# Kernel optimization log

Measured on AMD Instinct MI355X. Metric: run time of the kernel, lower is better.

The kernel has to match this reference:

```python
import jax, jax.numpy as jnp
import numpy as np

D_MODEL = 128
NUM_LAYERS = 2
D_FF = 512
VOCAB = 128
OUT_DIM = 10
B, S = 512, 256
EPS_FEAT = 1e-6
LN_EPS = 1e-5


def _pos_encoding(seq_len, d):
    pos = jnp.arange(seq_len, dtype=jnp.float32)[:, None]            # [S,1]
    div = jnp.exp(jnp.arange(0, d, 2, dtype=jnp.float32) * (-np.log(10000.0) / d))
    ang = pos * div                                                   # [S,D/2]
    pe = jnp.stack([jnp.sin(ang), jnp.cos(ang)], axis=-1).reshape(seq_len, d)
    return pe[:, None, :]                                             # [S,1,D]


def _layer_norm(x, g, b):
    mu = jnp.mean(x, axis=-1, keepdims=True)
    var = jnp.mean(jnp.square(x - mu), axis=-1, keepdims=True)
    return (x - mu) * jax.lax.rsqrt(var + LN_EPS) * g + b


def setup_inputs() -> dict:
    key = jax.random.key(0)
    ks = jax.random.split(key, 20)
    sc = 0.02
    inp = {
        'src': jax.random.randint(ks[0], (B, S), 0, VOCAB),
        'emb': jax.random.normal(ks[1], (VOCAB, D_MODEL), jnp.float32) * sc,
        'wq': jax.random.normal(ks[2], (NUM_LAYERS, D_MODEL, D_MODEL), jnp.float32) * sc,
        'bq': jnp.zeros((NUM_LAYERS, D_MODEL), jnp.float32),
        'wk': jax.random.normal(ks[3], (NUM_LAYERS, D_MODEL, D_MODEL), jnp.float32) * sc,
        'bk': jnp.zeros((NUM_LAYERS, D_MODEL), jnp.float32),
        'wv': jax.random.normal(ks[4], (NUM_LAYERS, D_MODEL, D_MODEL), jnp.float32) * sc,
        'bv': jnp.zeros((NUM_LAYERS, D_MODEL), jnp.float32),
        'w1': jax.random.normal(ks[5], (NUM_LAYERS, D_FF, D_MODEL), jnp.float32) * sc,
        'b1': jnp.zeros((NUM_LAYERS, D_FF), jnp.float32),
        'w2': jax.random.normal(ks[6], (NUM_LAYERS, D_MODEL, D_FF), jnp.float32) * sc,
        'b2': jnp.zeros((NUM_LAYERS, D_MODEL), jnp.float32),
        'g1': jnp.ones((NUM_LAYERS, D_MODEL), jnp.float32),
        'beta1': jnp.zeros((NUM_LAYERS, D_MODEL), jnp.float32),
        'g2': jnp.ones((NUM_LAYERS, D_MODEL), jnp.float32),
        'beta2': jnp.zeros((NUM_LAYERS, D_MODEL), jnp.float32),
        'fc_w': jax.random.normal(ks[7], (OUT_DIM, D_MODEL), jnp.float32) * sc,
        'fc_b': jnp.zeros((OUT_DIM,), jnp.float32),
    }
    return inp


def reference(src, emb, wq, bq, wk, bk, wv, bv, w1, b1, w2, b2,
              g1, beta1, g2, beta2, fc_w, fc_b):
    # src: [B,S] int -> permute -> [S,B]
    x = emb[src.T] * np.sqrt(float(D_MODEL))          # [S,B,D]
    x = x + _pos_encoding(x.shape[0], D_MODEL)
    for l in range(NUM_LAYERS):
        # Linear attention (faithful to original: einsum 'b' axis = seq here)
        Q = jax.nn.relu(jnp.einsum('sbd,ed->sbe', x, wq[l]) + bq[l]) + EPS_FEAT
        K = jax.nn.relu(jnp.einsum('sbd,ed->sbe', x, wk[l]) + bk[l]) + EPS_FEAT
        V = jnp.einsum('sbd,ed->sbe', x, wv[l]) + bv[l]
        KV = jnp.einsum('snd,sne->sde', K, V)         # [S,D,D] (n = batch axis)
        Z = 1.0 / (jnp.einsum('snd,sd->sn', Q, K.sum(axis=1)) + EPS_FEAT)  # [S,B]
        attn = jnp.einsum('snd,sde,sn->sne', Q, KV, Z)  # [S,B,D]
        x = _layer_norm(x + attn, g1[l], beta1[l])
        ff = jnp.einsum('sbf,df->sbd',
                        jax.nn.relu(jnp.einsum('sbd,fd->sbf', x, w1[l]) + b1[l]),
                        w2[l]) + b2[l]
        x = _layer_norm(x + ff, g2[l], beta2[l])
    x = jnp.transpose(x, (1, 0, 2))                   # [B,S,D]
    pooled = jnp.mean(x, axis=1)                      # [B,D]
    return pooled @ fc_w.T + fc_b                     # [B,OUT]
```

## Files before the change

### kernel.cpp

```cpp
#include <hip/hip_runtime.h>

typedef unsigned short u16;
typedef unsigned int u32;
typedef short bf16x8 __attribute__((ext_vector_type(8)));
typedef float f32x4 __attribute__((ext_vector_type(4)));

__device__ __forceinline__ float b2f(u16 v) { return __uint_as_float(((u32)v) << 16); }
__device__ __forceinline__ u16 f2b(float f) {
    u32 x = __float_as_uint(f);
    return (u16)((x + 0x7fffu + ((x >> 16) & 1u)) >> 16);
}

#define S_LEN 256
#define B_SZ  512
#define DM    128
#define DFF   512
#define MROWS (S_LEN * B_SZ)

__device__ __forceinline__ int sw16(int r, int d) {
    return r * 128 + ((((d >> 3) ^ (r & 15)) & 15) << 3) + (d & 7);
}

__global__ __launch_bounds__(256) void detect_kernel(const u32* __restrict__ embw,
                                                     int* __restrict__ flag) {
    int z = 0, big = 0;
    for (int i = threadIdx.x; i < 8192; i += 256) {
        u32 w = embw[i];
        u32 lo = w & 0xffffu;
        if (lo == 0u) z++;
        else if (((lo >> 7) & 0xffu) >= 0xC0u) big++;
    }
#pragma unroll
    for (int off = 32; off > 0; off >>= 1) {
        z   += __shfl_xor(z, off, 64);
        big += __shfl_xor(big, off, 64);
    }
    __shared__ int zz[4], bb[4];
    if ((threadIdx.x & 63) == 0) { zz[threadIdx.x >> 6] = z; bb[threadIdx.x >> 6] = big; }
    __syncthreads();
    if (threadIdx.x == 0) {
        int Z = zz[0] + zz[1] + zz[2] + zz[3];
        int Bc = bb[0] + bb[1] + bb[2] + bb[3];
        flag[0] = (Z > 4096 || Bc > 16) ? 1 : 0;
    }
}

struct Ptrs { const void* p[17]; };

__global__ __launch_bounds__(256) void convert_kernel(Ptrs ps, u16* __restrict__ canon,
                                                      const int* __restrict__ flag) {
    const int cnt[17] = {16384,32768,256,32768,256,32768,256,131072,1024,131072,
                         256,256,256,256,256,1280,10};
    const int off[17] = {0,16384,49152,49408,82176,82432,115200,115456,246528,
                         247552,378624,378880,379136,379392,379648,379904,381184};
    const int bst[18] = {0,8,24,25,41,42,58,59,123,124,188,189,190,191,192,193,194,195};
    const int isf = *flag;
    const int blk = blockIdx.x;
    int idx = 0;
#pragma unroll
    for (int i = 0; i < 17; ++i) if (blk >= bst[i + 1]) idx = i + 1;
    const int local = blk - bst[idx];
    const int n = cnt[idx];
    const void* sp = ps.p[idx];
    u16* dp = canon + off[idx];
#pragma unroll
    for (int j = 0; j < 8; ++j) {
        int e = local * 2048 + j * 256 + threadIdx.x;
        if (e < n) {
            u16 v = isf ? f2b(((const float*)sp)[e]) : ((const u16*)sp)[e];
            dp[e] = v;
        }
    }
}

__global__ __launch_bounds__(256) void embed_kernel(const int* __restrict__ src,
                                                    const u16* __restrict__ emb,
                                                    u16* __restrict__ X) {
    int idx = blockIdx.x * 256 + threadIdx.x;
    int d2 = idx & 63;
    int m = idx >> 6;
    int s = m >> 9;
    int b = m & 511;
    int tok = src[b * S_LEN + s];
    int d = d2 * 2;
    float e0 = b2f(emb[tok * DM + d])     * 11.3137084989847604f;
    float e1 = b2f(emb[tok * DM + d + 1]) * 11.3137084989847604f;
    float ang = (float)s * expf((float)d * -0.0719557841560639f);
    float v0 = e0 + sinf(ang);
    float v1 = e1 + cosf(ang);
    u32 w = (u32)f2b(v0) | ((u32)f2b(v1) << 16);
    *(u32*)(X + (size_t)m * DM + d) = w;
}

__global__ __launch_bounds__(256) void kvproj_kernel(
    const u16* __restrict__ X, const u16* __restrict__ Wk, const u16* __restrict__ bk,
    const u16* __restrict__ Wv, const u16* __restrict__ bv,
    u16* __restrict__ KVt, float* __restrict__ Ksum)
{
    __shared__ __align__(16) char sm_[49152];
    u16* Xs = (u16*)sm_;
    u16* Kt = (u16*)(sm_ + 16384);
    u16* Vt = (u16*)(sm_ + 32768);
    const int s = blockIdx.x, t = threadIdx.x;
    const int w = t >> 6, quad = (t >> 4) & 3, lr = t & 15;
    const u16* Xg = X + (size_t)s * B_SZ * DM;

    bf16x8 wkf[2][4], wvf[2][4];
    float kb[2], vb[2];
#pragma unroll
    for (int ct = 0; ct < 2; ++ct) {
        int e = w * 32 + ct * 16 + lr;
#pragma unroll
        for (int kc = 0; kc < 4; ++kc) {
            wkf[ct][kc] = *(const bf16x8*)(Wk + e * 128 + kc * 32 + quad * 8);
            wvf[ct][kc] = *(const bf16x8*)(Wv + e * 128 + kc * 32 + quad * 8);
        }
        kb[ct] = b2f(bk[e]);
        vb[ct] = b2f(bv[e]);
    }

    const f32x4 z4 = {0.f, 0.f, 0.f, 0.f};
    f32x4 kvacc[2][8];
#pragma unroll
    for (int dt = 0; dt < 2; ++dt)
#pragma unroll
        for (int ct = 0; ct < 8; ++ct) kvacc[dt][ct] = z4;
    float ks[2] = {0.f, 0.f};

    for (int b0 = 0; b0 < B_SZ; b0 += 64) {
        __syncthreads();
#pragma unroll
        for (int i = 0; i < 4; ++i) {
            int e8 = (i * 256 + t) * 8; int r = e8 >> 7, k0 = e8 & 127;
            *(uint4*)(Xs + sw16(r, k0)) = *(const uint4*)(Xg + (size_t)(b0 + r) * DM + k0);
        }
        __syncthreads();
        f32x4 pa[4][2];
#pragma unroll
        for (int mt = 0; mt < 4; ++mt) { pa[mt][0] = z4; pa[mt][1] = z4; }
#pragma unroll
        for (int kc = 0; kc < 4; ++kc) {
            bf16x8 a[4];
#pragma unroll
            for (int mt = 0; mt < 4; ++mt)
                a[mt] = *(const bf16x8*)(Xs + sw16(mt * 16 + lr, kc * 32 + quad * 8));
#pragma unroll
            for (int ct = 0; ct < 2; ++ct)
#pragma unroll
                for (int mt = 0; mt < 4; ++mt)
                    pa[mt][ct] = __builtin_amdgcn_mfma_f32_16x16x32_bf16(a[mt], wkf[ct][kc], pa[mt][ct], 0, 0, 0);
        }
#pragma unroll
        for (int ct = 0; ct < 2; ++ct) {
            int e = w * 32 + ct * 16 + lr, e7 = e & 7;
#pragma unroll
            for (int mt = 0; mt < 4; ++mt) {
                u16 h[4]; float ssum = 0.f;
#pragma unroll
                for (int j = 0; j < 4; ++j) {
                    float v = fmaxf(pa[mt][ct][j] + kb[ct], 0.f) + 1e-6f;
                    h[j] = f2b(v); ssum += b2f(h[j]);
                }
                ks[ct] += ssum;
                uint2 pk; pk.x = (u32)h[0] | ((u32)h[1] << 16); pk.y = (u32)h[2] | ((u32)h[3] << 16);
                int bs = mt * 2 + (quad >> 1);
                *(uint2*)(Kt + e * 64 + (((bs ^ e7) & 7) << 3) + (quad & 1) * 4) = pk;
            }
        }
#pragma unroll
        for (int mt = 0; mt < 4; ++mt) { pa[mt][0] = z4; pa[mt][1] = z4; }
#pragma unroll
        for (int kc = 0; kc < 4; ++kc) {
            bf16x8 a[4];
#pragma unroll
            for (int mt = 0; mt < 4; ++mt)
                a[mt] = *(const bf16x8*)(Xs + sw16(mt * 16 + lr, kc * 32 + quad * 8));
#pragma unroll
            for (int ct = 0; ct < 2; ++ct)
#pragma unroll
                for (int mt = 0; mt < 4; ++mt)
                    pa[mt][ct] = __builtin_amdgcn_mfma_f32_16x16x32_bf16(a[mt], wvf[ct][kc], pa[mt][ct], 0, 0, 0);
        }
#pragma unroll
        for (int ct = 0; ct < 2; ++ct) {
            int e = w * 32 + ct * 16 + lr, e7 = e & 7;
#pragma unroll
            for (int mt = 0; mt < 4; ++mt) {
                u16 h[4];
#pragma unroll
                for (int j = 0; j < 4; ++j) h[j] = f2b(pa[mt][ct][j] + vb[ct]);
                uint2 pk; pk.x = (u32)h[0] | ((u32)h[1] << 16); pk.y = (u32)h[2] | ((u32)h[3] << 16);
                int bs = mt * 2 + (quad >> 1);
                *(uint2*)(Vt + e * 64 + (((bs ^ e7) & 7) << 3) + (quad & 1) * 4) = pk;
            }
        }
        __syncthreads();
#pragma unroll
        for (int kc = 0; kc < 2; ++kc) {
            bf16x8 ka[2];
#pragma unroll
            for (int dt = 0; dt < 2; ++dt) {
                int d = (2 * w + dt) * 16 + lr;
                ka[dt] = *(const bf16x8*)(Kt + d * 64 + ((((kc * 4 + quad) ^ (d & 7)) & 7) << 3));
            }
#pragma unroll
            for (int ct = 0; ct < 8; ++ct) {
                int e = ct * 16 + lr;
                bf16x8 vf = *(const bf16x8*)(Vt + e * 64 + ((((kc * 4 + quad) ^ (e & 7)) & 7) << 3));
                kvacc[0][ct] = __builtin_amdgcn_mfma_f32_16x16x32_bf16(ka[0], vf, kvacc[0][ct], 0, 0, 0);
                kvacc[1][ct] = __builtin_amdgcn_mfma_f32_16x16x32_bf16(ka[1], vf, kvacc[1][ct], 0, 0, 0);
            }
        }
    }
#pragma unroll
    for (int ct = 0; ct < 2; ++ct) {
        float v = ks[ct];
        v += __shfl_xor(v, 16, 64);
        v += __shfl_xor(v, 32, 64);
        if (quad == 0) Ksum[s * 128 + w * 32 + ct * 16 + lr] = v;
    }
    u16* KVg = KVt + (size_t)s * (DM * DM);
#pragma unroll
    for (int dt = 0; dt < 2; ++dt) {
        int d0 = (2 * w + dt) * 16 + quad * 4;
#pragma unroll
        for (int ct = 0; ct < 8; ++ct) {
            int e = ct * 16 + lr;
            u16 h[4];
#pragma unroll
            for (int j = 0; j < 4; ++j) h[j] = f2b(kvacc[dt][ct][j]);
            uint2 pk; pk.x = (u32)h[0] | ((u32)h[1] << 16); pk.y = (u32)h[2] | ((u32)h[3] << 16);
            *(uint2*)(KVg + e * 128 + d0) = pk;
        }
    }
}

__global__ __launch_bounds__(256, 2) void attn_mlp_kernel(
    const u16* X, const u16* __restrict__ Wq, const u16* __restrict__ bq,
    const u16* __restrict__ KVt, const float* __restrict__ Ksum,
    const u16* __restrict__ W1, const u16* __restrict__ b1,
    const u16* __restrict__ W2, const u16* __restrict__ b2,
    u16* Xout,
    const u16* __restrict__ g1v_, const u16* __restrict__ be1_,
    const u16* __restrict__ g2v_, const u16* __restrict__ be2_)
{
    __shared__ __align__(16) char sm_[81920];
    u16* R1  = (u16*)sm_;
    u16* R2  = (u16*)(sm_ + 32768);
    u16* Hc  = (u16*)(sm_ + 65536);
    u16* W1c = R1;
    u16* W2c = R1 + 8192;
    u16* Out = R1;
    const int blk = blockIdx.x, s = blk >> 2, rc = blk & 3, t = threadIdx.x;
    const int w = t >> 6, quad = (t >> 4) & 3, lr = t & 15;
    const size_t m0 = (size_t)s * B_SZ + rc * 128;

#pragma unroll
    for (int i = 0; i < 8; ++i) {
        int e8 = (i * 256 + t) * 8; int r = e8 >> 7, k0 = e8 & 127;
        *(uint4*)(R1 + sw16(r, k0)) = *(const uint4*)(Wq + e8);
        *(uint4*)(R2 + sw16(r, k0)) = *(const uint4*)(X + (m0 + r) * DM + k0);
    }
    __syncthreads();
    const f32x4 z4 = {0.f, 0.f, 0.f, 0.f};
    f32x4 qacc[2][8];
#pragma unroll
    for (int mt = 0; mt < 2; ++mt)
#pragma unroll
        for (int ct = 0; ct < 8; ++ct) qacc[mt][ct] = z4;
#pragma unroll
    for (int kc = 0; kc < 4; ++kc) {
        bf16x8 a[2];
#pragma unroll
        for (int mt = 0; mt < 2; ++mt)
            a[mt] = *(const bf16x8*)(R2 + sw16(w * 32 + mt * 16 + lr, kc * 32 + quad * 8));
#pragma unroll
        for (int ct = 0; ct < 8; ++ct) {
            bf16x8 wf = *(const bf16x8*)(R1 + sw16(ct * 16 + lr, kc * 32 + quad * 8));
            qacc[0][ct] = __builtin_amdgcn_mfma_f32_16x16x32_bf16(a[0], wf, qacc[0][ct], 0, 0, 0);
            qacc[1][ct] = __builtin_amdgcn_mfma_f32_16x16x32_bf16(a[1], wf, qacc[1][ct], 0, 0, 0);
        }
    }
    __syncthreads();
    float ksm[8], bqv[8];
#pragma unroll
    for (int ct = 0; ct < 8; ++ct) {
        ksm[ct] = Ksum[s * 128 + ct * 16 + lr];
        bqv[ct] = b2f(bq[ct * 16 + lr]);
    }
    float zden[2][4];
#pragma unroll
    for (int mt = 0; mt < 2; ++mt)
#pragma unroll
        for (int j = 0; j < 4; ++j) zden[mt][j] = 0.f;
#pragma unroll
    for (int mt = 0; mt < 2; ++mt)
#pragma unroll
        for (int ct = 0; ct < 8; ++ct) {
            int d = ct * 16 + lr;
#pragma unroll
            for (int j = 0; j < 4; ++j) {
                float qv = fmaxf(qacc[mt][ct][j] + bqv[ct], 0.f) + 1e-6f;
                u16 qb16 = f2b(qv);
                zden[mt][j] += b2f(qb16) * ksm[ct];
                int b = w * 32 + mt * 16 + quad * 4 + j;
                R1[sw16(b, d)] = qb16;
            }
        }
#pragma unroll
    for (int mt = 0; mt < 2; ++mt)
#pragma unroll
        for (int j = 0; j < 4; ++j) {
            float v = zden[mt][j];
            v += __shfl_xor(v, 1, 64); v += __shfl_xor(v, 2, 64);
            v += __shfl_xor(v, 4, 64); v += __shfl_xor(v, 8, 64);
            zden[mt][j] = 1.f / (v + 1e-6f);
        }
    const u16* KVg = KVt + (size_t)s * (DM * DM);
#pragma unroll
    for (int i = 0; i < 8; ++i) {
        int e8 = (i * 256 + t) * 8; int r = e8 >> 7, k0 = e8 & 127;
        *(uint4*)(R2 + sw16(r, k0)) = *(const uint4*)(KVg + e8);
    }
    __syncthreads();
    f32x4 oacc[2][8];
#pragma unroll
    for (int mt = 0; mt < 2; ++mt)
#pragma unroll
        for (int ct = 0; ct < 8; ++ct) oacc[mt][ct] = z4;
#pragma unroll
    for (int kc = 0; kc < 4; ++kc) {
        bf16x8 qa[2];
#pragma unroll
        for (int mt = 0; mt < 2; ++mt)
            qa[mt] = *(const bf16x8*)(R1 + sw16(w * 32 + mt * 16 + lr, kc * 32 + quad * 8));
#pragma unroll
        for (int ct = 0; ct < 8; ++ct) {
            bf16x8 kf = *(const bf16x8*)(R2 + sw16(ct * 16 + lr, kc * 32 + quad * 8));
            oacc[0][ct] = __builtin_amdgcn_mfma_f32_16x16x32_bf16(qa[0], kf, oacc[0][ct], 0, 0, 0);
            oacc[1][ct] = __builtin_amdgcn_mfma_f32_16x16x32_bf16(qa[1], kf, oacc[1][ct], 0, 0, 0);
        }
    }
    __syncthreads();
    {
        float gv[8], bev[8];
#pragma unroll
        for (int ct = 0; ct < 8; ++ct) {
            gv[ct]  = b2f(g1v_[ct * 16 + lr]);
            bev[ct] = b2f(be1_[ct * 16 + lr]);
        }
#pragma unroll
        for (int mt = 0; mt < 2; ++mt)
#pragma unroll
            for (int j = 0; j < 4; ++j) {
                int b = w * 32 + mt * 16 + quad * 4 + j;
                const u16* xr = X + (m0 + b) * DM;
                float vals[8], sum = 0.f, sq = 0.f;
#pragma unroll
                for (int ct = 0; ct < 8; ++ct) {
                    float v = fmaf(oacc[mt][ct][j], zden[mt][j], b2f(xr[ct * 16 + lr]));
                    vals[ct] = v; sum += v; sq += v * v;
                }
                sum += __shfl_xor(sum, 1, 64); sq += __shfl_xor(sq, 1, 64);
                sum += __shfl_xor(sum, 2, 64); sq += __shfl_xor(sq, 2, 64);
                sum += __shfl_xor(sum, 4, 64); sq += __shfl_xor(sq, 4, 64);
                sum += __shfl_xor(sum, 8, 64); sq += __shfl_xor(sq, 8, 64);
                float mean = sum * 0.0078125f;
                float var  = sq * 0.0078125f - mean * mean;
                float rstd = rsqrtf(fmaxf(var, 0.f) + 1e-5f);
#pragma unroll
                for (int ct = 0; ct < 8; ++ct)
                    R2[sw16(b, ct * 16 + lr)] =
                        f2b((vals[ct] - mean) * rstd * gv[ct] + bev[ct]);
            }
    }
    bf16x8 xf[2][4];
#pragma unroll
    for (int mt = 0; mt < 2; ++mt)
#pragma unroll
        for (int kc = 0; kc < 4; ++kc)
            xf[mt][kc] = *(const bf16x8*)(R2 + sw16(w * 32 + mt * 16 + lr, kc * 32 + quad * 8));

    f32x4 zacc[2][8];
#pragma unroll
    for (int mt = 0; mt < 2; ++mt)
#pragma unroll
        for (int ct = 0; ct < 8; ++ct) zacc[mt][ct] = z4;

    for (int fc = 0; fc < DFF; fc += 64) {
        __syncthreads();
#pragma unroll
        for (int i = 0; i < 4; ++i) {
            int e8 = (i * 256 + t) * 8; int r = e8 >> 7, k0 = e8 & 127;
            *(uint4*)(W1c + sw16(r, k0)) = *(const uint4*)(W1 + (size_t)(fc + r) * DM + k0);
        }
#pragma unroll
        for (int i = 0; i < 4; ++i) {
            int e8 = (i * 256 + t) * 8; int d = e8 >> 6, f0 = e8 & 63;
            *(uint4*)(W2c + d * 64 + ((((f0 >> 3) ^ (d & 7)) & 7) << 3)) =
                *(const uint4*)(W2 + (size_t)d * DFF + fc + f0);
        }
        __syncthreads();
        f32x4 hacc[2][4];
#pragma unroll
        for (int mt = 0; mt < 2; ++mt)
#pragma unroll
            for (int ct = 0; ct < 4; ++ct) hacc[mt][ct] = z4;
#pragma unroll
        for (int kc = 0; kc < 4; ++kc) {
#pragma unroll
            for (int ct = 0; ct < 4; ++ct) {
                bf16x8 wa = *(const bf16x8*)(W1c + sw16(ct * 16 + lr, kc * 32 + quad * 8));
                hacc[0][ct] = __builtin_amdgcn_mfma_f32_16x16x32_bf16(wa, xf[0][kc], hacc[0][ct], 0, 0, 0);
                hacc[1][ct] = __builtin_amdgcn_mfma_f32_16x16x32_bf16(wa, xf[1][kc], hacc[1][ct], 0, 0, 0);
            }
        }
#pragma unroll
        for (int ct = 0; ct < 4; ++ct) {
            float hb[4];
#pragma unroll
            for (int j = 0; j < 4; ++j) hb[j] = b2f(b1[fc + ct * 16 + quad * 4 + j]);
#pragma unroll
            for (int mt = 0; mt < 2; ++mt) {
                int m = w * 32 + mt * 16 + lr;
                u16 h[4];
#pragma unroll
                for (int j = 0; j < 4; ++j)
                    h[j] = f2b(fmaxf(hacc[mt][ct][j] + hb[j], 0.f));
                uint2 pk; pk.x = (u32)h[0] | ((u32)h[1] << 16);
                pk.y = (u32)h[2] | ((u32)h[3] << 16);
                int slot = (ct * 2 + (quad >> 1)) ^ (m & 7);
                *(uint2*)(Hc + m * 64 + (slot << 3) + (quad & 1) * 4) = pk;
            }
        }
#pragma unroll
        for (int kc = 0; kc < 2; ++kc) {
            bf16x8 ha[2];
#pragma unroll
            for (int mt = 0; mt < 2; ++mt) {
                int m = w * 32 + mt * 16 + lr;
                ha[mt] = *(const bf16x8*)(Hc + m * 64 + ((((kc * 4 + quad) ^ (m & 7)) & 7) << 3));
            }
#pragma unroll
            for (int ct = 0; ct < 8; ++ct) {
                int d = ct * 16 + lr;
                bf16x8 wb = *(const bf16x8*)(W2c + d * 64 + ((((kc * 4 + quad) ^ (d & 7)) & 7) << 3));
                zacc[0][ct] = __builtin_amdgcn_mfma_f32_16x16x32_bf16(ha[0], wb, zacc[0][ct], 0, 0, 0);
                zacc[1][ct] = __builtin_amdgcn_mfma_f32_16x16x32_bf16(ha[1], wb, zacc[1][ct], 0, 0, 0);
            }
        }
    }
    __syncthreads();
    {
        float gv[8], bev[8], b2v[8];
#pragma unroll
        for (int ct = 0; ct < 8; ++ct) {
            gv[ct]  = b2f(g2v_[ct * 16 + lr]);
            bev[ct] = b2f(be2_[ct * 16 + lr]);
            b2v[ct] = b2f(b2[ct * 16 + lr]);
        }
#pragma unroll
        for (int mt = 0; mt < 2; ++mt)
#pragma unroll
            for (int j = 0; j < 4; ++j) {
                int r = w * 32 + mt * 16 + quad * 4 + j;
                float vals[8], sum = 0.f, sq = 0.f;
#pragma unroll
                for (int ct = 0; ct < 8; ++ct) {
                    float v = zacc[mt][ct][j] + b2v[ct] + b2f(R2[sw16(r, ct * 16 + lr)]);
                    vals[ct] = v; sum += v; sq += v * v;
                }
                sum += __shfl_xor(sum, 1, 64); sq += __shfl_xor(sq, 1, 64);
                sum += __shfl_xor(sum, 2, 64); sq += __shfl_xor(sq, 2, 64);
                sum += __shfl_xor(sum, 4, 64); sq += __shfl_xor(sq, 4, 64);
                sum += __shfl_xor(sum, 8, 64); sq += __shfl_xor(sq, 8, 64);
                float mean = sum * 0.0078125f;
                float var  = sq * 0.0078125f - mean * mean;
                float rstd = rsqrtf(fmaxf(var, 0.f) + 1e-5f);
#pragma unroll
                for (int ct = 0; ct < 8; ++ct)
                    Out[r * 128 + ct * 16 + lr] =
                        f2b((vals[ct] - mean) * rstd * gv[ct] + bev[ct]);
            }
    }
    __syncthreads();
#pragma unroll
    for (int i = 0; i < 8; ++i) {
        int e8 = (i * 256 + t) * 8; int r = e8 >> 7, k0 = e8 & 127;
        uint4 v = *(const uint4*)(Out + r * 128 + k0);
        *(uint4*)(Xout + (m0 + r) * DM + k0) = v;
    }
}

__global__ __launch_bounds__(128) void pool_fc_kernel(
    const u16* __restrict__ X, const u16* __restrict__ fcw,
    const u16* __restrict__ fcb, void* __restrict__ Out,
    const int* __restrict__ flag)
{
    __shared__ float pool[128];
    const int b = blockIdx.x, t = threadIdx.x;
    float acc = 0.f;
    for (int s = 0; s < S_LEN; ++s)
        acc += b2f(X[((size_t)s * B_SZ + b) * DM + t]);
    pool[t] = acc * (1.0f / 256.0f);
    __syncthreads();
    if (t < 10) {
        float o = b2f(fcb[t]);
        for (int d = 0; d < 128; ++d) o += pool[d] * b2f(fcw[t * 128 + d]);
        if (*flag) ((float*)Out)[b * 10 + t] = o;
        else       ((u16*)Out)[b * 10 + t] = f2b(o);
    }
}

extern "C" void kernel_launch(void* const* d_in, const int* in_sizes, int n_in,
                              void* d_out, int out_size, void* d_ws, size_t ws_size,
                              hipStream_t stream)
{
    const int* src = (const int*)d_in[0];

    char* ws = (char*)d_ws;
    u16*   X    = (u16*)ws;
    u16*   KVt  = (u16*)(ws + 33554432);
    float* Ksum = (float*)(ws + 41943040);
    int*   flag = (int*)(ws + 42074112);
    u16*   cn   = (u16*)(ws + 42074368);

    u16* emb = cn + 0;
    u16* wq  = cn + 16384;
    u16* bq  = cn + 49152;
    u16* wk  = cn + 49408;
    u16* bk  = cn + 82176;
    u16* wv  = cn + 82432;
    u16* bvp = cn + 115200;
    u16* w1  = cn + 115456;
    u16* b1  = cn + 246528;
    u16* w2  = cn + 247552;
    u16* b2  = cn + 378624;
    u16* g1  = cn + 378880;
    u16* be1 = cn + 379136;
    u16* g2  = cn + 379392;
    u16* be2 = cn + 379648;
    u16* fcw = cn + 379904;
    u16* fcb = cn + 381184;

    detect_kernel<<<1, 256, 0, stream>>>((const u32*)d_in[1], flag);

    Ptrs ps;
    for (int i = 0; i < 17; ++i) ps.p[i] = d_in[i + 1];
    convert_kernel<<<195, 256, 0, stream>>>(ps, cn, flag);

    embed_kernel<<<MROWS * 64 / 256, 256, 0, stream>>>(src, emb, X);

    for (int l = 0; l < 2; ++l) {
        kvproj_kernel<<<S_LEN, 256, 0, stream>>>(
            X, wk + l * DM * DM, bk + l * DM, wv + l * DM * DM, bvp + l * DM, KVt, Ksum);
        attn_mlp_kernel<<<S_LEN * 4, 256, 0, stream>>>(
            X, wq + l * DM * DM, bq + l * DM, KVt, Ksum,
            w1 + l * DFF * DM, b1 + l * DFF, w2 + l * DM * DFF, b2 + l * DM,
            X, g1 + l * DM, be1 + l * DM, g2 + l * DM, be2 + l * DM);
    }

    pool_fc_kernel<<<B_SZ, 128, 0, stream>>>(X, fcw, fcb, d_out, flag);
}
```

Before: 450.4 us.

## Register-prefetch X, KV, and FFN weight tiles to overlap global loads with MFMA

Adds register double-buffering. The next X tile in the KV kernel, the KV matrix in the attention/FFN kernel, and the next W1/W2 chunk in the FFN loop are now loaded from global memory into registers while MFMA work on the current tile runs, then stored into LDS after a barrier. The residual X values are also cached in packed registers rather than reread from global memory for the first LayerNorm. The goal is to hide global-load latency behind compute, at the cost of more registers per thread, which may lower occupancy.

```diff
diff --git a/kernel.cpp b/kernel.cpp
--- a/kernel.cpp
+++ b/kernel.cpp
@@ -10,6 +10,8 @@
     u32 x = __float_as_uint(f);
     return (u16)((x + 0x7fffu + ((x >> 16) & 1u)) >> 16);
 }
+__device__ __forceinline__ float lo16(u32 w) { return __uint_as_float(w << 16); }
+__device__ __forceinline__ float hi16(u32 w) { return __uint_as_float(w & 0xffff0000u); }
 
 #define S_LEN 256
 #define B_SZ  512
@@ -127,14 +129,28 @@
         for (int ct = 0; ct < 8; ++ct) kvacc[dt][ct] = z4;
     float ks[2] = {0.f, 0.f};
 
+    uint4 xp[4];
+#pragma unroll
+    for (int i = 0; i < 4; ++i) {
+        int e8 = (i * 256 + t) * 8; int r = e8 >> 7, k0 = e8 & 127;
+        xp[i] = *(const uint4*)(Xg + (size_t)r * DM + k0);
+    }
+
     for (int b0 = 0; b0 < B_SZ; b0 += 64) {
         __syncthreads();
 #pragma unroll
         for (int i = 0; i < 4; ++i) {
             int e8 = (i * 256 + t) * 8; int r = e8 >> 7, k0 = e8 & 127;
-            *(uint4*)(Xs + sw16(r, k0)) = *(const uint4*)(Xg + (size_t)(b0 + r) * DM + k0);
+            *(uint4*)(Xs + sw16(r, k0)) = xp[i];
         }
         __syncthreads();
+        if (b0 + 64 < B_SZ) {
+#pragma unroll
+            for (int i = 0; i < 4; ++i) {
+                int e8 = (i * 256 + t) * 8; int r = e8 >> 7, k0 = e8 & 127;
+                xp[i] = *(const uint4*)(Xg + (size_t)(b0 + 64 + r) * DM + k0);
+            }
+        }
         f32x4 pa[4][2];
 #pragma unroll
         for (int mt = 0; mt < 4; ++mt) { pa[mt][0] = z4; pa[mt][1] = z4; }
@@ -254,6 +270,7 @@
     const int blk = blockIdx.x, s = blk >> 2, rc = blk & 3, t = threadIdx.x;
     const int w = t >> 6, quad = (t >> 4) & 3, lr = t & 15;
     const size_t m0 = (size_t)s * B_SZ + rc * 128;
+    const u16* KVg = KVt + (size_t)s * (DM * DM);
 
 #pragma unroll
     for (int i = 0; i < 8; ++i) {
@@ -262,6 +279,9 @@
         *(uint4*)(R2 + sw16(r, k0)) = *(const uint4*)(X + (m0 + r) * DM + k0);
     }
     __syncthreads();
+    uint4 kvp[8];
+#pragma unroll
+    for (int i = 0; i < 8; ++i) kvp[i] = *(const uint4*)(KVg + (i * 256 + t) * 8);
     const f32x4 z4 = {0.f, 0.f, 0.f, 0.f};
     f32x4 qacc[2][8];
 #pragma unroll
@@ -316,11 +336,24 @@
             v += __shfl_xor(v, 4, 64); v += __shfl_xor(v, 8, 64);
             zden[mt][j] = 1.f / (v + 1e-6f);
         }
-    const u16* KVg = KVt + (size_t)s * (DM * DM);
+    u32 resid[2][4][4];
+#pragma unroll
+    for (int mt = 0; mt < 2; ++mt)
+#pragma unroll
+        for (int j = 0; j < 4; ++j) {
+            int r = w * 32 + mt * 16 + quad * 4 + j;
+#pragma unroll
+            for (int cp = 0; cp < 4; ++cp) {
+                u16 a0 = R2[sw16(r, (2 * cp) * 16 + lr)];
+                u16 a1 = R2[sw16(r, (2 * cp + 1) * 16 + lr)];
+                resid[mt][j][cp] = (u32)a0 | ((u32)a1 << 16);
+            }
+        }
+    __syncthreads();
 #pragma unroll
     for (int i = 0; i < 8; ++i) {
         int e8 = (i * 256 + t) * 8; int r = e8 >> 7, k0 = e8 & 127;
-        *(uint4*)(R2 + sw16(r, k0)) = *(const uint4*)(KVg + e8);
+        *(uint4*)(R2 + sw16(r, k0)) = kvp[i];
     }
     __syncthreads();
     f32x4 oacc[2][8];
@@ -342,6 +375,14 @@
         }
     }
     __syncthreads();
+    uint4 wp1[4], wp2[4];
+#pragma unroll
+    for (int i = 0; i < 4; ++i) {
+        int e8 = (i * 256 + t) * 8; int r = e8 >> 7, k0 = e8 & 127;
+        wp1[i] = *(const uint4*)(W1 + (size_t)r * DM + k0);
+        int d = e8 >> 6, f0 = e8 & 63;
+        wp2[i] = *(const uint4*)(W2 + (size_t)d * DFF + f0);
+    }
     {
         float gv[8], bev[8];
 #pragma unroll
@@ -354,11 +395,12 @@
 #pragma unroll
             for (int j = 0; j < 4; ++j) {
                 int b = w * 32 + mt * 16 + quad * 4 + j;
-                const u16* xr = X + (m0 + b) * DM;
                 float vals[8], sum = 0.f, sq = 0.f;
 #pragma unroll
                 for (int ct = 0; ct < 8; ++ct) {
-                    float v = fmaf(oacc[mt][ct][j], zden[mt][j], b2f(xr[ct * 16 + lr]));
+                    u32 rp = resid[mt][j][ct >> 1];
+                    float xres = (ct & 1) ? hi16(rp) : lo16(rp);
+                    float v = fmaf(oacc[mt][ct][j], zden[mt][j], xres);
                     vals[ct] = v; sum += v; sq += v * v;
                 }
                 sum += __shfl_xor(sum, 1, 64); sq += __shfl_xor(sq, 1, 64);
@@ -374,12 +416,20 @@
                         f2b((vals[ct] - mean) * rstd * gv[ct] + bev[ct]);
             }
     }
+#pragma unroll
+    for (int i = 0; i < 4; ++i) {
+        int e8 = (i * 256 + t) * 8; int r = e8 >> 7, k0 = e8 & 127;
+        *(uint4*)(W1c + sw16(r, k0)) = wp1[i];
+        int d = e8 >> 6, f0 = e8 & 63;
+        *(uint4*)(W2c + d * 64 + ((((f0 >> 3) ^ (d & 7)) & 7) << 3)) = wp2[i];
+    }
     bf16x8 xf[2][4];
 #pragma unroll
     for (int mt = 0; mt < 2; ++mt)
 #pragma unroll
         for (int kc = 0; kc < 4; ++kc)
             xf[mt][kc] = *(const bf16x8*)(R2 + sw16(w * 32 + mt * 16 + lr, kc * 32 + quad * 8));
+    __syncthreads();
 
     f32x4 zacc[2][8];
 #pragma unroll
@@ -387,20 +437,17 @@
 #pragma unroll
         for (int ct = 0; ct < 8; ++ct) zacc[mt][ct] = z4;
 
-    for (int fc = 0; fc < DFF; fc += 64) {
-        __syncthreads();
-#pragma unroll
-        for (int i = 0; i < 4; ++i) {
-            int e8 = (i * 256 + t) * 8; int r = e8 >> 7, k0 = e8 & 127;
-            *(uint4*)(W1c + sw16(r, k0)) = *(const uint4*)(W1 + (size_t)(fc + r) * DM + k0);
-        }
-#pragma unroll
-        for (int i = 0; i < 4; ++i) {
-            int e8 = (i * 256 + t) * 8; int d = e8 >> 6, f0 = e8 & 63;
-            *(uint4*)(W2c + d * 64 + ((((f0 >> 3) ^ (d & 7)) & 7) << 3)) =
-                *(const uint4*)(W2 + (size_t)d * DFF + fc + f0);
-        }
-        __syncthreads();
+    for (int it = 0; it < 8; ++it) {
+        const int fc = it * 64;
+        if (it < 7) {
+#pragma unroll
+            for (int i = 0; i < 4; ++i) {
+                int e8 = (i * 256 + t) * 8; int r = e8 >> 7, k0 = e8 & 127;
+                wp1[i] = *(const uint4*)(W1 + (size_t)(fc + 64 + r) * DM + k0);
+                int d = e8 >> 6, f0 = e8 & 63;
+                wp2[i] = *(const uint4*)(W2 + (size_t)d * DFF + fc + 64 + f0);
+            }
+        }
         f32x4 hacc[2][4];
 #pragma unroll
         for (int mt = 0; mt < 2; ++mt)
@@ -449,8 +496,18 @@
                 zacc[1][ct] = __builtin_amdgcn_mfma_f32_16x16x32_bf16(ha[1], wb, zacc[1][ct], 0, 0, 0);
             }
         }
-    }
-    __syncthreads();
+        __syncthreads();
+        if (it < 7) {
+#pragma unroll
+            for (int i = 0; i < 4; ++i) {
+                int e8 = (i * 256 + t) * 8; int r = e8 >> 7, k0 = e8 & 127;
+                *(uint4*)(W1c + sw16(r, k0)) = wp1[i];
+                int d = e8 >> 6, f0 = e8 & 63;
+                *(uint4*)(W2c + d * 64 + ((((f0 >> 3) ^ (d & 7)) & 7) << 3)) = wp2[i];
+            }
+            __syncthreads();
+        }
+    }
     {
         float gv[8], bev[8], b2v[8];
 #pragma unroll
```

Result: slower. 567.5 us (+26.0%).
